# Performance work log

Hardware: AMD Instinct MI355X
Metric: run time of the kernel (lower is better)

Reference implementation:

```python
import jax, jax.numpy as jnp
import numpy as np

D_MODEL = 1024
NUM_HEAD = 16
HEAD_DIM = D_MODEL // NUM_HEAD  # 64


def setup_inputs() -> dict:
    key = jax.random.key(0)
    ks = jax.random.split(key, 9)
    B, S = 2, 2048
    s = 0.02
    return {
        "x": jax.random.normal(ks[0], (B, S, D_MODEL), dtype=jnp.float32),
        "Wq": jax.random.normal(ks[1], (D_MODEL, D_MODEL), dtype=jnp.float32) * s,
        "bq": jax.random.normal(ks[2], (D_MODEL,), dtype=jnp.float32) * s,
        "Wk": jax.random.normal(ks[3], (D_MODEL, D_MODEL), dtype=jnp.float32) * s,
        "bk": jax.random.normal(ks[4], (D_MODEL,), dtype=jnp.float32) * s,
        "Wv": jax.random.normal(ks[5], (D_MODEL, D_MODEL), dtype=jnp.float32) * s,
        "bv": jax.random.normal(ks[6], (D_MODEL,), dtype=jnp.float32) * s,
        "Wo": jax.random.normal(ks[7], (D_MODEL, D_MODEL), dtype=jnp.float32) * s,
        "bo": jax.random.normal(ks[8], (D_MODEL,), dtype=jnp.float32) * s,
    }


def _split_head(t):
    # [B,S,D] -> [B,H,S,hd]
    B, S, _ = t.shape
    return t.reshape(B, S, NUM_HEAD, HEAD_DIM).transpose(0, 2, 1, 3)


def reference(x, Wq, bq, Wk, bk, Wv, bv, Wo, bo):
    B, S, D = x.shape
    q = _split_head(x @ Wq.T + bq)  # [B,H,S,hd]
    k = _split_head(x @ Wk.T + bk)
    v = _split_head(x @ Wv.T + bv)
    scale = 1.0 / jnp.sqrt(jnp.asarray(HEAD_DIM, dtype=x.dtype))
    scores = jnp.einsum("bhqd,bhkd->bhqk", q, k) * scale  # [B,H,S,S]
    attn = jax.nn.softmax(scores, axis=-1)
    out = jnp.einsum("bhqk,bhkd->bhqd", attn, v)  # [B,H,S,hd]
    out = out.transpose(0, 2, 1, 3).reshape(B, S, D)
    return out @ Wo.T + bo
```

## Files before the change

kernel.cpp:

```cpp
#include <hip/hip_runtime.h>
#include <cstdint>


typedef unsigned short ush;
typedef __bf16 bf16x8 __attribute__((ext_vector_type(8)));
typedef float f32x4 __attribute__((ext_vector_type(4)));
typedef ush u16x8 __attribute__((ext_vector_type(8)));
typedef ush u16x4 __attribute__((ext_vector_type(4)));
typedef unsigned int u32x4 __attribute__((ext_vector_type(4)));

__device__ __forceinline__ ush f2bf(float f) {
  unsigned int u = __float_as_uint(f);
  u += 0x7fffu + ((u >> 16) & 1u);
  return (ush)(u >> 16);
}

__device__ __forceinline__ unsigned int pack2bf_ru(float a, float b) {
  unsigned int ua = __float_as_uint(a) + 0x8000u;
  unsigned int ub = __float_as_uint(b) + 0x8000u;
  return __builtin_amdgcn_perm(ub, ua, 0x07060302u);
}

__device__ __forceinline__ bf16x8 bc8(u16x8 v) {
  return __builtin_bit_cast(bf16x8, v);
}

__device__ __forceinline__ void async16(const void* g, void* l) {
  __builtin_amdgcn_global_load_lds(
      (const __attribute__((address_space(1))) unsigned int*)(uintptr_t)g,
      (__attribute__((address_space(3))) unsigned int*)(uintptr_t)l, 16, 0, 0);
}

__global__ __launch_bounds__(256) void convert_kernel(
    const float* __restrict__ x, const float* __restrict__ Wq,
    const float* __restrict__ Wk, const float* __restrict__ Wv,
    const float* __restrict__ Wo,
    ush* __restrict__ xb, ush* __restrict__ Wqb, ush* __restrict__ Wkb,
    ush* __restrict__ Wvb, ush* __restrict__ Wob)
{
  int tid = blockIdx.x * 256 + threadIdx.x;
  int base = tid * 4;
  const float* src; ush* dst; int idx;
  if (base < 4194304) { src = x; dst = xb; idx = base; }
  else {
    int r = base - 4194304;
    int seg = r >> 20;
    idx = r & 1048575;
    src = seg == 0 ? Wq : seg == 1 ? Wk : seg == 2 ? Wv : Wo;
    dst = seg == 0 ? Wqb : seg == 1 ? Wkb : seg == 2 ? Wvb : Wob;
  }
  float4 f = *(const float4*)(src + idx);
  u16x4 u = { f2bf(f.x), f2bf(f.y), f2bf(f.z), f2bf(f.w) };
  *(u16x4*)(dst + idx) = u;
}

__device__ __forceinline__ void gemm128_core(
    const ush* __restrict__ gA, const ush* __restrict__ gB,
    int m0, int n0, ush* lA, ush* lB, f32x4 (&acc)[4][4])
{
  const int t = threadIdx.x, w = t >> 6, lane = t & 63;
  const int l15 = lane & 15, quad = lane >> 4;
  const int wm = (w >> 1) * 64, wn = (w & 1) * 64;
#pragma unroll
  for (int i = 0; i < 4; ++i)
#pragma unroll
    for (int j = 0; j < 4; ++j) acc[i][j] = (f32x4){0.f, 0.f, 0.f, 0.f};

  for (int kt = 0; kt < 1024; kt += 64) {
#pragma unroll
    for (int i = 0; i < 4; ++i) {
      int j = i * 256 + w * 64 + lane;
      int row = j >> 3, cc = (j & 7) ^ (row & 7);
      async16(gA + (size_t)(m0 + row) * 1024 + kt + cc * 8,
              lA + (i * 256 + w * 64) * 8);
    }
#pragma unroll
    for (int i = 0; i < 4; ++i) {
      int j = i * 256 + w * 64 + lane;
      int row = j >> 3, cc = (j & 7) ^ (row & 7);
      async16(gB + (size_t)(n0 + row) * 1024 + kt + cc * 8,
              lB + (i * 256 + w * 64) * 8);
    }
    __syncthreads();
#pragma unroll
    for (int kf = 0; kf < 2; ++kf) {
      bf16x8 aF[4], bF[4];
#pragma unroll
      for (int mt = 0; mt < 4; ++mt) {
        int row = wm + mt * 16 + l15;
        aF[mt] = bc8(*(const u16x8*)(lA + row * 64 + (((kf * 4 + quad) ^ (row & 7)) * 8)));
      }
#pragma unroll
      for (int nt = 0; nt < 4; ++nt) {
        int row = wn + nt * 16 + l15;
        bF[nt] = bc8(*(const u16x8*)(lB + row * 64 + (((kf * 4 + quad) ^ (row & 7)) * 8)));
      }
#pragma unroll
      for (int mt = 0; mt < 4; ++mt)
#pragma unroll
        for (int nt = 0; nt < 4; ++nt)
          acc[mt][nt] = __builtin_amdgcn_mfma_f32_16x16x32_bf16(
              aF[mt], bF[nt], acc[mt][nt], 0, 0, 0);
    }
    __syncthreads();
  }
}

__global__ __launch_bounds__(256, 2) void qkv_gemm(
    const ush* __restrict__ xb, const ush* __restrict__ Wqb,
    const ush* __restrict__ Wkb, const ush* __restrict__ Wvb,
    const float* __restrict__ bq, const float* __restrict__ bk,
    const float* __restrict__ bv,
    ush* __restrict__ q, ush* __restrict__ k, ush* __restrict__ vt)
{
  int bid = blockIdx.x;
  int wsel = bid >> 8;
  int rem = bid & 255;
  int m0 = (rem & 31) * 128;
  int n0 = (rem >> 5) * 128;
  const ush* gB = wsel == 0 ? Wqb : wsel == 1 ? Wkb : Wvb;
  const float* bias = wsel == 0 ? bq : wsel == 1 ? bk : bv;
  const float oscale = wsel == 1 ? 0.180336880f : 1.0f;

  __shared__ alignas(16) ush lA[128 * 64];
  __shared__ alignas(16) ush lB[128 * 64];
  f32x4 acc[4][4];
  gemm128_core(xb, gB, m0, n0, lA, lB, acc);

  const int t = threadIdx.x, w = t >> 6, lane = t & 63;
  const int l15 = lane & 15, quad = lane >> 4;
  const int wm = (w >> 1) * 64, wn = (w & 1) * 64;
  if (wsel == 2) {
#pragma unroll
    for (int nt = 0; nt < 4; ++nt) {
      int o = n0 + wn + nt * 16 + l15;
      float bl = bias[o];
      int h = o >> 6, d = o & 63;
#pragma unroll
      for (int mt = 0; mt < 4; ++mt) {
        int tb = m0 + wm + mt * 16 + quad * 4;
        int b = tb >> 11, s = tb & 2047;
        int so = s & 63;
        int sp = (s & ~63) | (so & 35) | ((so & 12) << 1) | ((so & 16) >> 2);
        u16x4 pk = { f2bf(acc[mt][nt][0] + bl), f2bf(acc[mt][nt][1] + bl),
                     f2bf(acc[mt][nt][2] + bl), f2bf(acc[mt][nt][3] + bl) };
        *(u16x4*)(vt + (size_t)(((b * 16 + h) * 64) + d) * 2048 + sp) = pk;
      }
    }
  } else {
    ush* dst = wsel == 0 ? q : k;
#pragma unroll
    for (int nt = 0; nt < 4; ++nt) {
      int o = n0 + wn + nt * 16 + l15;
      float bl = bias[o];
      int h = o >> 6, d = o & 63;
#pragma unroll
      for (int mt = 0; mt < 4; ++mt)
#pragma unroll
        for (int r = 0; r < 4; ++r) {
          int token = m0 + wm + mt * 16 + quad * 4 + r;
          int b = token >> 11, s = token & 2047;
          dst[(size_t)(((b * 16 + h) * 2048) + s) * 64 + d] =
              f2bf((acc[mt][nt][r] + bl) * oscale);
        }
    }
  }
}

__global__ __launch_bounds__(128, 2) void attn_kernel(
    const ush* __restrict__ Q, const ush* __restrict__ K,
    const ush* __restrict__ VT, ush* __restrict__ O)
{
  const int bid = blockIdx.x;
  const int bh = (bid & 7) * 4 + (bid >> 8);
  const int qt = (bid >> 3) & 31;
  const ush* qb = Q + (size_t)bh * 2048 * 64;
  const ush* kb = K + (size_t)bh * 2048 * 64;
  const ush* vtb = VT + (size_t)bh * 64 * 2048;
  const int t = threadIdx.x, w = t >> 6, lane = t & 63;
  const int l15 = lane & 15, quad = lane >> 4;
  const int q0 = qt * 64;

  __shared__ alignas(16) ush lK[2][64 * 64];
  __shared__ alignas(16) ush lV[2][64 * 64];

  const int r0 = t >> 3;
  const int c0 = (t & 7) ^ (r0 & 7);
  const ush* kSrc = kb + (size_t)r0 * 64 + c0 * 8;
  const ush* vSrc = vtb + (size_t)r0 * 2048 + c0 * 8;

  bf16x8 qF[4][2];
#pragma unroll
  for (int g = 0; g < 4; ++g)
#pragma unroll
    for (int kf = 0; kf < 2; ++kf)
      qF[g][kf] = bc8(*(const u16x8*)(qb + (size_t)(q0 + g * 16 + l15) * 64 +
                                      kf * 32 + quad * 8));

  float li[4] = {0.f, 0.f, 0.f, 0.f};
  f32x4 accO[4][4];
#pragma unroll
  for (int g = 0; g < 4; ++g)
#pragma unroll
    for (int dt = 0; dt < 4; ++dt) accO[g][dt] = (f32x4){0.f, 0.f, 0.f, 0.f};

#pragma unroll
  for (int i = 0; i < 4; ++i) {
    async16(kSrc + i * 1024, lK[0] + (i * 128 + t) * 8);
    async16(vSrc + (size_t)i * 16 * 2048, lV[0] + (i * 128 + t) * 8);
  }
  __syncthreads();

  for (int it = 0; it < 32; ++it) {
    const int cur = it & 1, nxt = cur ^ 1;
    if (it + 1 < 32) {
      const size_t ko = (size_t)(it + 1) * 64 * 64;
      const int vo = (it + 1) * 64;
#pragma unroll
      for (int i = 0; i < 4; ++i) {
        async16(kSrc + ko + i * 1024, lK[nxt] + (i * 128 + t) * 8);
        async16(vSrc + vo + (size_t)i * 16 * 2048, lV[nxt] + (i * 128 + t) * 8);
      }
    }
    const ush* lk = lK[cur];
    const ush* lv = lV[cur];

    f32x4 sc[4][2];
#pragma unroll
    for (int g = 0; g < 4; ++g)
#pragma unroll
      for (int mt = 0; mt < 2; ++mt) sc[g][mt] = (f32x4){0.f, 0.f, 0.f, 0.f};
#pragma unroll
    for (int kf = 0; kf < 2; ++kf) {
#pragma unroll
      for (int mt = 0; mt < 2; ++mt) {
        int row = (2 * w + mt) * 16 + l15;
        bf16x8 aK = bc8(*(const u16x8*)(lk + row * 64 + (((kf * 4 + quad) ^ (row & 7)) * 8)));
#pragma unroll
        for (int g = 0; g < 4; ++g)
          sc[g][mt] = __builtin_amdgcn_mfma_f32_16x16x32_bf16(
              aK, qF[g][kf], sc[g][mt], 0, 0, 0);
      }
    }

#pragma unroll
    for (int g = 0; g < 4; ++g) {
      float rs = 0.f;
#pragma unroll
      for (int mt = 0; mt < 2; ++mt)
#pragma unroll
        for (int r = 0; r < 4; ++r) {
          sc[g][mt][r] = __builtin_amdgcn_exp2f(sc[g][mt][r]);
          rs += sc[g][mt][r];
        }
      rs += __shfl_xor(rs, 16);
      rs += __shfl_xor(rs, 32);
      li[g] += rs;
    }

    bf16x8 aV[4];
#pragma unroll
    for (int dt = 0; dt < 4; ++dt)
      aV[dt] = bc8(*(const u16x8*)(lv + (dt * 16 + l15) * 64 +
                                   (((w * 4 + quad) ^ (l15 & 7)) * 8)));
#pragma unroll
    for (int g = 0; g < 4; ++g) {
      u32x4 bw = { pack2bf_ru(sc[g][0][0], sc[g][0][1]),
                   pack2bf_ru(sc[g][0][2], sc[g][0][3]),
                   pack2bf_ru(sc[g][1][0], sc[g][1][1]),
                   pack2bf_ru(sc[g][1][2], sc[g][1][3]) };
      bf16x8 bP = __builtin_bit_cast(bf16x8, bw);
#pragma unroll
      for (int dt = 0; dt < 4; ++dt)
        accO[g][dt] = __builtin_amdgcn_mfma_f32_16x16x32_bf16(
            aV[dt], bP, accO[g][dt], 0, 0, 0);
    }
    __syncthreads();
  }

  float* redO = (float*)lK;
  float* redL = (float*)lV;
#define SEND_GROUP(G)                                                        \
  {                                                                          \
    _Pragma("unroll")                                                        \
    for (int dt = 0; dt < 4; ++dt)                                           \
      *(f32x4*)(redO + (((G) * 4 + dt) * 64 + lane) * 4) = accO[G][dt];      \
    redL[(G) * 64 + lane] = li[G];                                           \
  }
  if (w == 0) { SEND_GROUP(2); SEND_GROUP(3); }
  else        { SEND_GROUP(0); SEND_GROUP(1); }
  __syncthreads();
  const int b = bh >> 4, h = bh & 15;
#define FINISH_GROUP(G)                                                      \
  {                                                                          \
    _Pragma("unroll")                                                        \
    for (int dt = 0; dt < 4; ++dt)                                           \
      accO[G][dt] += *(const f32x4*)(redO + (((G) * 4 + dt) * 64 + lane) * 4);\
    float lsum = li[G] + redL[(G) * 64 + lane];                              \
    const float linv = __builtin_amdgcn_rcpf(lsum);                          \
    const int s = q0 + (G) * 16 + l15;                                       \
    _Pragma("unroll")                                                        \
    for (int dt = 0; dt < 4; ++dt) {                                         \
      u16x4 pk = { f2bf(accO[G][dt][0] * linv), f2bf(accO[G][dt][1] * linv), \
                   f2bf(accO[G][dt][2] * linv), f2bf(accO[G][dt][3] * linv) };\
      *(u16x4*)(O + (size_t)(b * 2048 + s) * 1024 + h * 64 + dt * 16 +       \
                quad * 4) = pk;                                              \
    }                                                                        \
  }
  if (w == 0) { FINISH_GROUP(0); FINISH_GROUP(1); }
  else        { FINISH_GROUP(2); FINISH_GROUP(3); }
#undef SEND_GROUP
#undef FINISH_GROUP
}

__global__ __launch_bounds__(256, 2) void out_gemm(
    const ush* __restrict__ ab, const ush* __restrict__ Wob,
    const float* __restrict__ bo, float* __restrict__ out)
{
  int rem = blockIdx.x;
  int m0 = (rem & 31) * 128;
  int n0 = (rem >> 5) * 128;
  __shared__ alignas(16) ush lA[128 * 64];
  __shared__ alignas(16) ush lB[128 * 64];
  f32x4 acc[4][4];
  gemm128_core(ab, Wob, m0, n0, lA, lB, acc);

  const int t = threadIdx.x, w = t >> 6, lane = t & 63;
  const int l15 = lane & 15, quad = lane >> 4;
  const int wm = (w >> 1) * 64, wn = (w & 1) * 64;
#pragma unroll
  for (int nt = 0; nt < 4; ++nt) {
    int o = n0 + wn + nt * 16 + l15;
    float bl = bo[o];
#pragma unroll
    for (int mt = 0; mt < 4; ++mt)
#pragma unroll
      for (int r = 0; r < 4; ++r) {
        int token = m0 + wm + mt * 16 + quad * 4 + r;
        out[(size_t)token * 1024 + o] = acc[mt][nt][r] + bl;
      }
  }
}

extern "C" void kernel_launch(void* const* d_in, const int* in_sizes, int n_in,
                              void* d_out, int out_size, void* d_ws, size_t ws_size,
                              hipStream_t stream)
{
  const float* x  = (const float*)d_in[0];
  const float* Wq = (const float*)d_in[1];
  const float* bq = (const float*)d_in[2];
  const float* Wk = (const float*)d_in[3];
  const float* bk = (const float*)d_in[4];
  const float* Wv = (const float*)d_in[5];
  const float* bv = (const float*)d_in[6];
  const float* Wo = (const float*)d_in[7];
  const float* bo = (const float*)d_in[8];
  float* out = (float*)d_out;

  char* ws = (char*)d_ws;
  ush* xb  = (ush*)(ws);
  ush* Wqb = (ush*)(ws + (size_t)( 8u << 20));
  ush* Wkb = (ush*)(ws + (size_t)(10u << 20));
  ush* Wvb = (ush*)(ws + (size_t)(12u << 20));
  ush* Wob = (ush*)(ws + (size_t)(14u << 20));
  ush* qb  = (ush*)(ws + (size_t)(16u << 20));
  ush* kb  = (ush*)(ws + (size_t)(24u << 20));
  ush* vtb = (ush*)(ws + (size_t)(32u << 20));
  ush* ab  = (ush*)(ws + (size_t)(40u << 20));

  convert_kernel<<<8192, 256, 0, stream>>>(x, Wq, Wk, Wv, Wo,
                                           xb, Wqb, Wkb, Wvb, Wob);
  qkv_gemm<<<768, 256, 0, stream>>>(xb, Wqb, Wkb, Wvb, bq, bk, bv, qb, kb, vtb);
  attn_kernel<<<1024, 128, 0, stream>>>(qb, kb, vtb, ab);
  out_gemm<<<256, 256, 0, stream>>>(ab, Wob, bo, out);
}
```

Measured before the change: 185.5 us.

## Split attention block into four waves sharing K/V tiles across query halves

The attention kernel moves from 128 to 256 threads per block. Two wave pairs each handle 32 of the 64 query rows while sharing the same double-buffered K/V LDS tiles, so the per-wave accumulator and score register footprint is halved and launch bounds allow more waves per CU. The row-sum cross-lane shuffles are moved out of the inner loop and done once after it. This trades fewer registers and more latency hiding for more waves contending on the LDS reads of the K/V tiles.

Measured after the change: 184.3 us. No clear change (-0.6%).

```diff
diff --git a/kernel.cpp b/kernel.cpp
--- a/kernel.cpp
+++ b/kernel.cpp
@@ -167,7 +167,7 @@
   }
 }
 
-__global__ __launch_bounds__(128, 2) void attn_kernel(
+__global__ __launch_bounds__(256, 4) void attn_kernel(
     const ush* __restrict__ Q, const ush* __restrict__ K,
     const ush* __restrict__ VT, ush* __restrict__ O)
 {
@@ -178,8 +178,9 @@
   const ush* kb = K + (size_t)bh * 2048 * 64;
   const ush* vtb = VT + (size_t)bh * 64 * 2048;
   const int t = threadIdx.x, w = t >> 6, lane = t & 63;
+  const int wk = w & 1, wq = w >> 1;
   const int l15 = lane & 15, quad = lane >> 4;
-  const int q0 = qt * 64;
+  const int q0 = qt * 64 + wq * 32;
 
   __shared__ alignas(16) ush lK[2][64 * 64];
   __shared__ alignas(16) ush lV[2][64 * 64];
@@ -189,25 +190,25 @@
   const ush* kSrc = kb + (size_t)r0 * 64 + c0 * 8;
   const ush* vSrc = vtb + (size_t)r0 * 2048 + c0 * 8;
 
-  bf16x8 qF[4][2];
-#pragma unroll
-  for (int g = 0; g < 4; ++g)
+  bf16x8 qF[2][2];
+#pragma unroll
+  for (int g = 0; g < 2; ++g)
 #pragma unroll
     for (int kf = 0; kf < 2; ++kf)
       qF[g][kf] = bc8(*(const u16x8*)(qb + (size_t)(q0 + g * 16 + l15) * 64 +
                                       kf * 32 + quad * 8));
 
-  float li[4] = {0.f, 0.f, 0.f, 0.f};
-  f32x4 accO[4][4];
-#pragma unroll
-  for (int g = 0; g < 4; ++g)
+  float li[2] = {0.f, 0.f};
+  f32x4 accO[2][4];
+#pragma unroll
+  for (int g = 0; g < 2; ++g)
 #pragma unroll
     for (int dt = 0; dt < 4; ++dt) accO[g][dt] = (f32x4){0.f, 0.f, 0.f, 0.f};
 
 #pragma unroll
-  for (int i = 0; i < 4; ++i) {
-    async16(kSrc + i * 1024, lK[0] + (i * 128 + t) * 8);
-    async16(vSrc + (size_t)i * 16 * 2048, lV[0] + (i * 128 + t) * 8);
+  for (int i = 0; i < 2; ++i) {
+    async16(kSrc + i * 2048, lK[0] + (i * 256 + t) * 8);
+    async16(vSrc + (size_t)i * 32 * 2048, lV[0] + (i * 256 + t) * 8);
   }
   __syncthreads();
 
@@ -217,34 +218,34 @@
       const size_t ko = (size_t)(it + 1) * 64 * 64;
       const int vo = (it + 1) * 64;
 #pragma unroll
-      for (int i = 0; i < 4; ++i) {
-        async16(kSrc + ko + i * 1024, lK[nxt] + (i * 128 + t) * 8);
-        async16(vSrc + vo + (size_t)i * 16 * 2048, lV[nxt] + (i * 128 + t) * 8);
+      for (int i = 0; i < 2; ++i) {
+        async16(kSrc + ko + i * 2048, lK[nxt] + (i * 256 + t) * 8);
+        async16(vSrc + vo + (size_t)i * 32 * 2048, lV[nxt] + (i * 256 + t) * 8);
       }
     }
     const ush* lk = lK[cur];
     const ush* lv = lV[cur];
 
-    f32x4 sc[4][2];
-#pragma unroll
-    for (int g = 0; g < 4; ++g)
+    f32x4 sc[2][2];
+#pragma unroll
+    for (int g = 0; g < 2; ++g)
 #pragma unroll
       for (int mt = 0; mt < 2; ++mt) sc[g][mt] = (f32x4){0.f, 0.f, 0.f, 0.f};
 #pragma unroll
     for (int kf = 0; kf < 2; ++kf) {
 #pragma unroll
       for (int mt = 0; mt < 2; ++mt) {
-        int row = (2 * w + mt) * 16 + l15;
+        int row = (2 * wk + mt) * 16 + l15;
         bf16x8 aK = bc8(*(const u16x8*)(lk + row * 64 + (((kf * 4 + quad) ^ (row & 7)) * 8)));
 #pragma unroll
-        for (int g = 0; g < 4; ++g)
+        for (int g = 0; g < 2; ++g)
           sc[g][mt] = __builtin_amdgcn_mfma_f32_16x16x32_bf16(
               aK, qF[g][kf], sc[g][mt], 0, 0, 0);
       }
     }
 
 #pragma unroll
-    for (int g = 0; g < 4; ++g) {
+    for (int g = 0; g < 2; ++g) {
       float rs = 0.f;
 #pragma unroll
       for (int mt = 0; mt < 2; ++mt)
@@ -253,8 +254,6 @@
           sc[g][mt][r] = __builtin_amdgcn_exp2f(sc[g][mt][r]);
           rs += sc[g][mt][r];
         }
-      rs += __shfl_xor(rs, 16);
-      rs += __shfl_xor(rs, 32);
       li[g] += rs;
     }
 
@@ -262,9 +261,9 @@
 #pragma unroll
     for (int dt = 0; dt < 4; ++dt)
       aV[dt] = bc8(*(const u16x8*)(lv + (dt * 16 + l15) * 64 +
-                                   (((w * 4 + quad) ^ (l15 & 7)) * 8)));
-#pragma unroll
-    for (int g = 0; g < 4; ++g) {
+                                   (((wk * 4 + quad) ^ (l15 & 7)) * 8)));
+#pragma unroll
+    for (int g = 0; g < 2; ++g) {
       u32x4 bw = { pack2bf_ru(sc[g][0][0], sc[g][0][1]),
                    pack2bf_ru(sc[g][0][2], sc[g][0][3]),
                    pack2bf_ru(sc[g][1][0], sc[g][1][1]),
@@ -278,37 +277,43 @@
     __syncthreads();
   }
 
+#pragma unroll
+  for (int g = 0; g < 2; ++g) {
+    li[g] += __shfl_xor(li[g], 16);
+    li[g] += __shfl_xor(li[g], 32);
+  }
+
   float* redO = (float*)lK;
   float* redL = (float*)lV;
-#define SEND_GROUP(G)                                                        \
+  const int b = bh >> 4, h = bh & 15;
+#define SEND_GROUP(GL)                                                       \
   {                                                                          \
+    const int Gs = 2 * wq + (GL);                                            \
     _Pragma("unroll")                                                        \
     for (int dt = 0; dt < 4; ++dt)                                           \
-      *(f32x4*)(redO + (((G) * 4 + dt) * 64 + lane) * 4) = accO[G][dt];      \
-    redL[(G) * 64 + lane] = li[G];                                           \
-  }
-  if (w == 0) { SEND_GROUP(2); SEND_GROUP(3); }
-  else        { SEND_GROUP(0); SEND_GROUP(1); }
-  __syncthreads();
-  const int b = bh >> 4, h = bh & 15;
-#define FINISH_GROUP(G)                                                      \
+      *(f32x4*)(redO + ((Gs * 4 + dt) * 64 + lane) * 4) = accO[GL][dt];      \
+    redL[Gs * 64 + lane] = li[GL];                                           \
+  }
+#define FINISH_GROUP(GL)                                                     \
   {                                                                          \
+    const int Gf = 2 * wq + (GL);                                            \
     _Pragma("unroll")                                                        \
     for (int dt = 0; dt < 4; ++dt)                                           \
-      accO[G][dt] += *(const f32x4*)(redO + (((G) * 4 + dt) * 64 + lane) * 4);\
-    float lsum = li[G] + redL[(G) * 64 + lane];                              \
+      accO[GL][dt] += *(const f32x4*)(redO + ((Gf * 4 + dt) * 64 + lane) * 4);\
+    float lsum = li[GL] + redL[Gf * 64 + lane];                              \
     const float linv = __builtin_amdgcn_rcpf(lsum);                          \
-    const int s = q0 + (G) * 16 + l15;                                       \
+    const int s = q0 + (GL) * 16 + l15;                                      \
     _Pragma("unroll")                                                        \
     for (int dt = 0; dt < 4; ++dt) {                                         \
-      u16x4 pk = { f2bf(accO[G][dt][0] * linv), f2bf(accO[G][dt][1] * linv), \
-                   f2bf(accO[G][dt][2] * linv), f2bf(accO[G][dt][3] * linv) };\
+      u16x4 pk = { f2bf(accO[GL][dt][0] * linv), f2bf(accO[GL][dt][1] * linv),\
+                   f2bf(accO[GL][dt][2] * linv), f2bf(accO[GL][dt][3] * linv)};\
       *(u16x4*)(O + (size_t)(b * 2048 + s) * 1024 + h * 64 + dt * 16 +       \
                 quad * 4) = pk;                                              \
     }                                                                        \
   }
-  if (w == 0) { FINISH_GROUP(0); FINISH_GROUP(1); }
-  else        { FINISH_GROUP(2); FINISH_GROUP(3); }
+  if (wk == 0) { SEND_GROUP(1); } else { SEND_GROUP(0); }
+  __syncthreads();
+  if (wk == 0) { FINISH_GROUP(0); } else { FINISH_GROUP(1); }
 #undef SEND_GROUP
 #undef FINISH_GROUP
 }
@@ -371,6 +376,6 @@
   convert_kernel<<<8192, 256, 0, stream>>>(x, Wq, Wk, Wv, Wo,
                                            xb, Wqb, Wkb, Wvb, Wob);
   qkv_gemm<<<768, 256, 0, stream>>>(xb, Wqb, Wkb, Wvb, bq, bk, bv, qb, kb, vtb);
-  attn_kernel<<<1024, 128, 0, stream>>>(qb, kb, vtb, ab);
+  attn_kernel<<<1024, 256, 0, stream>>>(qb, kb, vtb, ab);
   out_gemm<<<256, 256, 0, stream>>>(ab, Wob, bo, out);
 }
```
